# Kernel tuning notes

Measured on AMD Instinct MI355X. Metric: run time of the kernel, lower is better.

## Reference

```python
import jax, jax.numpy as jnp
import numpy as np

B, HID = 32768, 128
NU = 0.49                 # poisson_ratio default
LAM_PHYS, LAM_EL = 0.1, 0.05
EPS = 1e-7


def setup_inputs() -> dict:
    key = jax.random.key(0)
    ks = jax.random.split(key, 8)
    def w(k, shape, fan_in):
        return jax.random.normal(k, shape, jnp.float32) / np.float32(np.sqrt(fan_in))
    return {
        "coords": jax.random.normal(ks[0], (B, 3), jnp.float32),
        "target_labels": jax.random.uniform(ks[1], (B, 1), jnp.float32),
        "target_stiffness": jax.random.uniform(ks[2], (B, 1), jnp.float32) * 10.0,
        "W1": w(ks[3], (3, HID), 3), "b1": jnp.zeros((HID,), jnp.float32),
        "W2": w(ks[4], (HID, HID), HID), "b2": jnp.zeros((HID,), jnp.float32),
        "Wp": w(ks[5], (HID, 1), HID), "bp": jnp.zeros((1,), jnp.float32),
        "Ws": w(ks[6], (HID, 1), HID), "bs": jnp.zeros((1,), jnp.float32),
        "Wd": w(ks[7], (HID, 3), HID), "bd": jnp.zeros((3,), jnp.float32),
    }


def reference(coords, target_labels, target_stiffness,
              W1, b1, W2, b2, Wp, bp, Ws, bs, Wd, bd):
    def feats(x):  # x: (...,3) -> (...,HID)
        h = jnp.tanh(x @ W1 + b1)
        return jnp.tanh(h @ W2 + b2)

    h = feats(coords)                                   # (B,HID)
    prediction = jax.nn.sigmoid(h @ Wp + bp)            # (B,1)
    stiffness = jax.nn.softplus(h @ Ws + bs)            # (B,1) Young's modulus E

    # displacement field u(x): R^3 -> R^3, pointwise
    def disp_fn(x):  # (3,) -> (3,)
        return feats(x) @ Wd + bd

    # Per-point Hessian H[b,i,j,k] = d2 u_i / dx_j dx_k  (B,3,3,3)
    Hm = jax.vmap(jax.jacfwd(jax.jacfwd(disp_fn)))(coords)
    laplacian = jnp.einsum('bijj->bi', Hm)              # (B,3) lap(u_i)
    grad_div = jnp.einsum('biik->bk', Hm)               # (B,3) grad(div u)

    # Lame parameters from E (matches torch code incl. nu_denom clamp)
    mu = stiffness / (2.0 * (1.0 + NU))
    nu_denom = max(1.0 - 2.0 * NU, 1e-5)
    lmbda = stiffness * NU / ((1.0 + NU) * nu_denom)
    residual = mu * laplacian + (lmbda + mu) * grad_div  # (B,3)
    phys_loss = jnp.mean(jnp.sum(residual ** 2, axis=-1))

    # BCE on clamped prediction/labels
    p = jnp.clip(prediction, EPS, 1.0 - EPS)
    t = jnp.clip(target_labels, 0.0, 1.0)
    bce = -jnp.mean(t * jnp.log(p) + (1.0 - t) * jnp.log(1.0 - p))
    data_loss = bce + 0.5 * jnp.mean((stiffness - target_stiffness) ** 2)

    elastic_loss = jnp.mean(jax.nn.relu(-stiffness) + jax.nn.relu(stiffness - 15.0))

    total = data_loss + LAM_PHYS * phys_loss + LAM_EL * elastic_loss
    raw_losses = jnp.stack([data_loss, phys_loss, elastic_loss])
    return total, raw_losses
```

## Files before the change

kernel.cpp:

```cpp
#include <hip/hip_runtime.h>
#include <math.h>

#define HIDN 128
#define NPTS 32768
#define PTS_PER_BLK 16
#define NBLK (NPTS / PTS_PER_BLK)

#define MU_COEF 0.33557046979865773f
#define LM_COEF 16.442953020134228f

typedef float f32x4  __attribute__((ext_vector_type(4)));
typedef short bf16x8 __attribute__((ext_vector_type(8)));


__device__ __forceinline__ unsigned short f2bf(float f) {
    unsigned u = __builtin_bit_cast(unsigned, f);
    u += 0x7fffu + ((u >> 16) & 1u);
    return (unsigned short)(u >> 16);
}

__device__ __forceinline__ float tanh_fast(float x) {
    float e = __builtin_amdgcn_exp2f(x * 2.885390081777927f);
    return 1.0f - 2.0f * __builtin_amdgcn_rcpf(e + 1.0f);
}

__global__ void prep_kernel(const float* __restrict__ W1,
                            const float* __restrict__ b1,
                            const float* __restrict__ W2,
                            float* __restrict__ ws)
{
    float* accum = ws;
    float* tab   = ws + 128;
    unsigned short* W2bf = (unsigned short*)(ws + 2048);
    int tid = blockIdx.x * blockDim.x + threadIdx.x;
    if (tid < 8) accum[tid] = 0.0f;
    if (tid < HIDN) {
        float w0 = W1[0 * HIDN + tid];
        float w1 = W1[1 * HIDN + tid];
        float w2 = W1[2 * HIDN + tid];
        float* t = tab + tid * 12;
        t[0] = w0; t[1] = w1; t[2] = w2; t[3] = b1[tid];
        t[4] = w0 * w0; t[5] = w0 * w1; t[6] = w0 * w2;
        t[7] = w1 * w1; t[8] = w1 * w2; t[9] = w2 * w2;
        t[10] = 0.0f; t[11] = 0.0f;
    }
    for (int i = tid; i < HIDN * HIDN; i += gridDim.x * blockDim.x) {
        int m = i >> 7, h = i & 127;
        W2bf[m * HIDN + h] = f2bf(W2[h * HIDN + m]);
    }
}

__global__ __launch_bounds__(256, 3) void pinn_main(
    const float* __restrict__ coords,
    const float* __restrict__ labels,
    const float* __restrict__ tstiff,
    const float* __restrict__ b2,
    const float* __restrict__ Wp, const float* __restrict__ bp,
    const float* __restrict__ Wsv, const float* __restrict__ bs,
    const float* __restrict__ Wd,
    const float* __restrict__ ws_ro,
    float* __restrict__ accum)
{
    const float* tab = ws_ro + 128;
    const unsigned short* W2bf = (const unsigned short*)(ws_ro + 2048);

    __shared__ __align__(16) char smem[43584];
    unsigned short* A  = (unsigned short*)smem;
    float*          red  = (float*)smem;
    float*          red2 = (float*)(smem + 43520);

    const int tid  = threadIdx.x;
    const int wave = __builtin_amdgcn_readfirstlane(tid >> 6);
    const int lane = tid & 63;
    const int blk  = blockIdx.x;

    {
        const int b  = tid & 15;
        const int hc = tid >> 4;
        const int h0 = hc * 8;
        const int gb = blk * PTS_PER_BLK + b;
        const float x0 = coords[gb * 3 + 0];
        const float x1 = coords[gb * 3 + 1];
        const float x2 = coords[gb * 3 + 2];
        unsigned pk[10][4];
#pragma unroll
        for (int i = 0; i < 8; ++i) {
            const float* t = tab + (h0 + i) * 12;
            float z = fmaf(x0, t[0], fmaf(x1, t[1], fmaf(x2, t[2], t[3])));
            float a  = tanh_fast(z);
            float g  = fmaf(-a, a, 1.0f);
            float ag = a * g;
            float c[10];
            c[0] = a;
            c[1] = g * t[0]; c[2] = g * t[1]; c[3] = g * t[2];
            c[4] = ag * t[4]; c[5] = ag * t[5]; c[6] = ag * t[6];
            c[7] = ag * t[7]; c[8] = ag * t[8]; c[9] = ag * t[9];
#pragma unroll
            for (int ch = 0; ch < 10; ++ch) {
                unsigned v = f2bf(c[ch]);
                if ((i & 1) == 0) pk[ch][i >> 1] = v;
                else              pk[ch][i >> 1] |= v << 16;
            }
        }
#pragma unroll
        for (int ch = 0; ch < 10; ++ch) {
            uint4* dst = (uint4*)(A + ch * (16 * 136) + b * 136 + h0);
            *dst = make_uint4(pk[ch][0], pk[ch][1], pk[ch][2], pk[ch][3]);
        }
    }
    __syncthreads();

    const int l = lane & 15;
    const int q = lane >> 4;

    f32x4 acc[10][2] = {};
#pragma unroll
    for (int ks = 0; ks < 4; ++ks) {
        const int hk = ks * 32 + q * 8;
        bf16x8 bfr[2];
#pragma unroll
        for (int mt = 0; mt < 2; ++mt) {
            const int m = wave * 32 + mt * 16 + l;
            bfr[mt] = *(const bf16x8*)(W2bf + m * HIDN + hk);
        }
#pragma unroll
        for (int ch = 0; ch < 10; ++ch) {
            bf16x8 afr = *(const bf16x8*)(A + ch * (16 * 136) + l * 136 + hk);
            acc[ch][0] = __builtin_amdgcn_mfma_f32_16x16x32_bf16(afr, bfr[0], acc[ch][0], 0, 0, 0);
            acc[ch][1] = __builtin_amdgcn_mfma_f32_16x16x32_bf16(afr, bfr[1], acc[ch][1], 0, 0, 0);
        }
    }

    float sum[4][8] = {};
#pragma unroll
    for (int mt = 0; mt < 2; ++mt) {
        const int m = wave * 32 + mt * 16 + l;
        const float wd0 = Wd[m * 3 + 0];
        const float wd1 = Wd[m * 3 + 1];
        const float wd2 = Wd[m * 3 + 2];
        const float wp  = Wp[m];
        const float wsv = Wsv[m];
        const float b2v = b2[m];
#pragma unroll
        for (int r = 0; r < 4; ++r) {
            const float z2 = acc[0][mt][r] + b2v;
            const float a2 = tanh_fast(z2);
            const float g2 = fmaf(-a2, a2, 1.0f);
            const float d2 = -2.0f * a2 * g2;
            const float t0 = acc[1][mt][r], t1 = acc[2][mt][r], t2 = acc[3][mt][r];
            const float q00 = acc[4][mt][r], q01 = acc[5][mt][r], q02 = acc[6][mt][r];
            const float q11 = acc[7][mt][r], q12 = acc[8][mt][r], q22 = acc[9][mt][r];
            const float qtr = q00 + q11 + q22;
            const float tt  = t0 * t0 + t1 * t1 + t2 * t2;
            const float Lm  = fmaf(-2.0f * g2, qtr, d2 * tt);
            const float wt  = wd0 * t0 + wd1 * t1 + wd2 * t2;
            const float m2g2 = -2.0f * g2;
            const float dwt  = d2 * wt;
            const float r0 = wd0 * q00 + wd1 * q01 + wd2 * q02;
            const float r1 = wd0 * q01 + wd1 * q11 + wd2 * q12;
            const float r2 = wd0 * q02 + wd1 * q12 + wd2 * q22;
            sum[r][0] += wp  * a2;
            sum[r][1] += wsv * a2;
            sum[r][2] += wd0 * Lm;
            sum[r][3] += wd1 * Lm;
            sum[r][4] += wd2 * Lm;
            sum[r][5] += m2g2 * r0 + dwt * t0;
            sum[r][6] += m2g2 * r1 + dwt * t1;
            sum[r][7] += m2g2 * r2 + dwt * t2;
        }
    }
    __syncthreads();

#pragma unroll
    for (int r = 0; r < 4; ++r) {
        const int b = q * 4 + r;
        const int slot = wave * 16 + l;
        float4* dst = (float4*)(red + (b * 64 + slot) * 8);
        dst[0] = make_float4(sum[r][0], sum[r][1], sum[r][2], sum[r][3]);
        dst[1] = make_float4(sum[r][4], sum[r][5], sum[r][6], sum[r][7]);
    }
    __syncthreads();

    {
        const int b  = tid >> 4;
        const int l2 = tid & 15;
        float v[8] = {};
#pragma unroll
        for (int w = 0; w < 4; ++w) {
            const float4* src = (const float4*)(red + (b * 64 + w * 16 + l2) * 8);
            float4 p0 = src[0], p1 = src[1];
            v[0] += p0.x; v[1] += p0.y; v[2] += p0.z; v[3] += p0.w;
            v[4] += p1.x; v[5] += p1.y; v[6] += p1.z; v[7] += p1.w;
        }
#pragma unroll
        for (int k = 0; k < 8; ++k) {
            v[k] += __shfl_xor(v[k], 1);
            v[k] += __shfl_xor(v[k], 2);
            v[k] += __shfl_xor(v[k], 4);
            v[k] += __shfl_xor(v[k], 8);
        }
        float bce_t = 0.f, sq_t = 0.f, phys_t = 0.f, el_t = 0.f;
        if (l2 == 0) {
            const int gb = blk * PTS_PER_BLK + b;
            const float fzp = v[0] + bp[0];
            const float fzs = v[1] + bs[0];
            float pred = 1.0f / (1.0f + expf(-fzp));
            pred = fminf(fmaxf(pred, 1e-7f), 1.0f - 1e-7f);
            const float E = fmaxf(fzs, 0.0f) + log1pf(expf(-fabsf(fzs)));
            const float mu = E * MU_COEF;
            const float cc = E * LM_COEF + mu;
            const float rr0 = mu * v[2] + cc * v[5];
            const float rr1 = mu * v[3] + cc * v[6];
            const float rr2 = mu * v[4] + cc * v[7];
            phys_t = rr0 * rr0 + rr1 * rr1 + rr2 * rr2;
            float tl = labels[gb];
            tl = fminf(fmaxf(tl, 0.0f), 1.0f);
            bce_t = -(tl * logf(pred) + (1.0f - tl) * logf(1.0f - pred));
            const float dsv = E - tstiff[gb];
            sq_t = dsv * dsv;
            el_t = fmaxf(-E, 0.0f) + fmaxf(E - 15.0f, 0.0f);
        }
#pragma unroll
        for (int m = 16; m < 64; m <<= 1) {
            bce_t  += __shfl_xor(bce_t, m);
            sq_t   += __shfl_xor(sq_t, m);
            phys_t += __shfl_xor(phys_t, m);
            el_t   += __shfl_xor(el_t, m);
        }
        if (lane == 0) {
            red2[wave * 4 + 0] = bce_t;
            red2[wave * 4 + 1] = sq_t;
            red2[wave * 4 + 2] = phys_t;
            red2[wave * 4 + 3] = el_t;
        }
    }
    __syncthreads();
    if (tid < 4) {
        float s = red2[0 * 4 + tid] + red2[1 * 4 + tid] + red2[2 * 4 + tid] + red2[3 * 4 + tid];
        atomicAdd(accum + tid, s);
    }
}

__global__ void finalize_kernel(const float* __restrict__ accum,
                                float* __restrict__ out)
{
    if (threadIdx.x == 0 && blockIdx.x == 0) {
        const float invB = 1.0f / (float)NPTS;
        const float bce  = accum[0] * invB;
        const float data = bce + 0.5f * accum[1] * invB;
        const float phys = accum[2] * invB;
        const float el   = accum[3] * invB;
        out[0] = data + 0.1f * phys + 0.05f * el;
        out[1] = data;
        out[2] = phys;
        out[3] = el;
    }
}

extern "C" void kernel_launch(void* const* d_in, const int* in_sizes, int n_in,
                              void* d_out, int out_size, void* d_ws, size_t ws_size,
                              hipStream_t stream)
{
    const float* coords = (const float*)d_in[0];
    const float* labels = (const float*)d_in[1];
    const float* tstiff = (const float*)d_in[2];
    const float* W1  = (const float*)d_in[3];
    const float* b1  = (const float*)d_in[4];
    const float* W2  = (const float*)d_in[5];
    const float* b2  = (const float*)d_in[6];
    const float* Wp  = (const float*)d_in[7];
    const float* bp  = (const float*)d_in[8];
    const float* Wsv = (const float*)d_in[9];
    const float* bs  = (const float*)d_in[10];
    const float* Wd  = (const float*)d_in[11];

    float* ws  = (float*)d_ws;
    float* out = (float*)d_out;

    prep_kernel<<<64, 256, 0, stream>>>(W1, b1, W2, ws);
    pinn_main<<<NBLK, 256, 0, stream>>>(coords, labels, tstiff, b2,
                                        Wp, bp, Wsv, bs, Wd, ws, ws);
    finalize_kernel<<<1, 64, 0, stream>>>(ws, out);
}
```

Measured before the change: 117.1 us.

## Fold first-layer weights into W2 variants to shrink per-point MFMA A operands

Moves the W1-dependent factors (w_j, |w|^2, Wd·w products) into nine precomputed bf16 B matrices, so each point needs only three A channels (a, g, a*g) instead of ten. The main kernel now handles 64 points per block, uses an XOR-swizzled LDS layout, loops over output column chunks, and fuses finalization into the last block via an atomic counter. This cuts per-point activation work and LDS traffic but adds more MFMAs per point (9 vs 10 per m-tile with larger tiles) and more global B-matrix reads, and it lowers occupancy to 2 blocks per CU. Extra bf16 rounding of the folded weights may change accuracy.

```diff
diff --git a/kernel.cpp b/kernel.cpp
--- a/kernel.cpp
+++ b/kernel.cpp
@@ -3,8 +3,8 @@
 
 #define HIDN 128
 #define NPTS 32768
-#define PTS_PER_BLK 16
-#define NBLK (NPTS / PTS_PER_BLK)
+#define PTSB 64
+#define NBLK (NPTS / PTSB)
 
 #define MU_COEF 0.33557046979865773f
 #define LM_COEF 16.442953020134228f
@@ -27,30 +27,39 @@
 __global__ void prep_kernel(const float* __restrict__ W1,
                             const float* __restrict__ b1,
                             const float* __restrict__ W2,
+                            const float* __restrict__ Wd,
                             float* __restrict__ ws)
 {
-    float* accum = ws;
-    float* tab   = ws + 128;
-    unsigned short* W2bf = (unsigned short*)(ws + 2048);
-    int tid = blockIdx.x * blockDim.x + threadIdx.x;
-    if (tid < 8) accum[tid] = 0.0f;
-    if (tid < HIDN) {
-        float w0 = W1[0 * HIDN + tid];
-        float w1 = W1[1 * HIDN + tid];
-        float w2 = W1[2 * HIDN + tid];
-        float* t = tab + tid * 12;
-        t[0] = w0; t[1] = w1; t[2] = w2; t[3] = b1[tid];
-        t[4] = w0 * w0; t[5] = w0 * w1; t[6] = w0 * w2;
-        t[7] = w1 * w1; t[8] = w1 * w2; t[9] = w2 * w2;
-        t[10] = 0.0f; t[11] = 0.0f;
-    }
-    for (int i = tid; i < HIDN * HIDN; i += gridDim.x * blockDim.x) {
-        int m = i >> 7, h = i & 127;
-        W2bf[m * HIDN + h] = f2bf(W2[h * HIDN + m]);
-    }
-}
-
-__global__ __launch_bounds__(256, 3) void pinn_main(
+    const int idx = blockIdx.x * blockDim.x + threadIdx.x;
+    const int h = idx & 127;
+    const int m = idx >> 7;
+    if (idx < 8) ws[idx] = 0.0f;
+    const float w0 = W1[0 * HIDN + h];
+    const float w1 = W1[1 * HIDN + h];
+    const float w2 = W1[2 * HIDN + h];
+    if (idx < 128) {
+        float4* tab4 = (float4*)(ws + 16);
+        tab4[h] = make_float4(w0, w1, w2, b1[h]);
+    }
+    const float W2v = W2[h * HIDN + m];
+    const float kap = w0 * Wd[m * 3 + 0] + w1 * Wd[m * 3 + 1] + w2 * Wd[m * 3 + 2];
+    const float s   = w0 * w0 + w1 * w1 + w2 * w2;
+    unsigned short* BM = (unsigned short*)((char*)ws + 4096);
+    const int o = m * HIDN + h;
+    BM[0 * 16384 + o] = f2bf(W2v);
+    BM[1 * 16384 + o] = f2bf(W2v * w0);
+    BM[2 * 16384 + o] = f2bf(W2v * w1);
+    BM[3 * 16384 + o] = f2bf(W2v * w2);
+    BM[4 * 16384 + o] = f2bf(W2v * kap);
+    BM[5 * 16384 + o] = f2bf(W2v * s);
+    BM[6 * 16384 + o] = f2bf(W2v * w0 * kap);
+    BM[7 * 16384 + o] = f2bf(W2v * w1 * kap);
+    BM[8 * 16384 + o] = f2bf(W2v * w2 * kap);
+}
+
+__constant__ int AIDX_[9] = {0, 1, 1, 1, 1, 2, 2, 2, 2};
+
+__global__ __launch_bounds__(256, 2) void pinn_main(
     const float* __restrict__ coords,
     const float* __restrict__ labels,
     const float* __restrict__ tstiff,
@@ -59,201 +68,206 @@
     const float* __restrict__ Wsv, const float* __restrict__ bs,
     const float* __restrict__ Wd,
     const float* __restrict__ ws_ro,
-    float* __restrict__ accum)
+    float* __restrict__ accum,
+    float* __restrict__ out)
 {
-    const float* tab = ws_ro + 128;
-    const unsigned short* W2bf = (const unsigned short*)(ws_ro + 2048);
-
-    __shared__ __align__(16) char smem[43584];
+    const float4* tab4 = (const float4*)(ws_ro + 16);
+    const unsigned short* BM = (const unsigned short*)((const char*)ws_ro + 4096);
+
+    __shared__ __align__(16) char smem[57344];
     unsigned short* A  = (unsigned short*)smem;
-    float*          red  = (float*)smem;
-    float*          red2 = (float*)(smem + 43520);
-
-    const int tid  = threadIdx.x;
-    const int wave = __builtin_amdgcn_readfirstlane(tid >> 6);
-    const int lane = tid & 63;
+    float*          red = (float*)(smem + 49152);
+
+    const int t    = threadIdx.x;
+    const int w    = __builtin_amdgcn_readfirstlane(t >> 6);
+    const int lane = t & 63;
+    const int l    = lane & 15;
+    const int q    = lane >> 4;
     const int blk  = blockIdx.x;
 
     {
-        const int b  = tid & 15;
-        const int hc = tid >> 4;
-        const int h0 = hc * 8;
-        const int gb = blk * PTS_PER_BLK + b;
+        float4* r4 = (float4*)red;
+        r4[t * 2 + 0] = make_float4(0.f, 0.f, 0.f, 0.f);
+        r4[t * 2 + 1] = make_float4(0.f, 0.f, 0.f, 0.f);
+    }
+
+    {
+        const int b  = t & 63;
+        const int gb = blk * PTSB + b;
         const float x0 = coords[gb * 3 + 0];
         const float x1 = coords[gb * 3 + 1];
         const float x2 = coords[gb * 3 + 2];
-        unsigned pk[10][4];
-#pragma unroll
-        for (int i = 0; i < 8; ++i) {
-            const float* t = tab + (h0 + i) * 12;
-            float z = fmaf(x0, t[0], fmaf(x1, t[1], fmaf(x2, t[2], t[3])));
-            float a  = tanh_fast(z);
-            float g  = fmaf(-a, a, 1.0f);
-            float ag = a * g;
-            float c[10];
-            c[0] = a;
-            c[1] = g * t[0]; c[2] = g * t[1]; c[3] = g * t[2];
-            c[4] = ag * t[4]; c[5] = ag * t[5]; c[6] = ag * t[6];
-            c[7] = ag * t[7]; c[8] = ag * t[8]; c[9] = ag * t[9];
-#pragma unroll
-            for (int ch = 0; ch < 10; ++ch) {
-                unsigned v = f2bf(c[ch]);
-                if ((i & 1) == 0) pk[ch][i >> 1] = v;
-                else              pk[ch][i >> 1] |= v << 16;
-            }
-        }
-#pragma unroll
-        for (int ch = 0; ch < 10; ++ch) {
-            uint4* dst = (uint4*)(A + ch * (16 * 136) + b * 136 + h0);
-            *dst = make_uint4(pk[ch][0], pk[ch][1], pk[ch][2], pk[ch][3]);
+#pragma unroll
+        for (int i = 0; i < 4; ++i) {
+            const int c = w * 4 + i;
+            unsigned pk[3][4];
+#pragma unroll
+            for (int hh = 0; hh < 8; ++hh) {
+                float4 tv = tab4[c * 8 + hh];
+                float z  = fmaf(x0, tv.x, fmaf(x1, tv.y, fmaf(x2, tv.z, tv.w)));
+                float a  = tanh_fast(z);
+                float g  = fmaf(-a, a, 1.0f);
+                float ag = a * g;
+                unsigned va = f2bf(a), vg = f2bf(g), vag = f2bf(ag);
+                if ((hh & 1) == 0) { pk[0][hh >> 1] = va; pk[1][hh >> 1] = vg; pk[2][hh >> 1] = vag; }
+                else { pk[0][hh >> 1] |= va << 16; pk[1][hh >> 1] |= vg << 16; pk[2][hh >> 1] |= vag << 16; }
+            }
+            const int dst = b * 128 + ((c ^ (b & 15)) * 8);
+#pragma unroll
+            for (int ch = 0; ch < 3; ++ch)
+                *(uint4*)(A + ch * 8192 + dst) = make_uint4(pk[ch][0], pk[ch][1], pk[ch][2], pk[ch][3]);
         }
     }
     __syncthreads();
 
-    const int l = lane & 15;
-    const int q = lane >> 4;
-
-    f32x4 acc[10][2] = {};
-#pragma unroll
-    for (int ks = 0; ks < 4; ++ks) {
-        const int hk = ks * 32 + q * 8;
-        bf16x8 bfr[2];
-#pragma unroll
-        for (int mt = 0; mt < 2; ++mt) {
-            const int m = wave * 32 + mt * 16 + l;
-            bfr[mt] = *(const bf16x8*)(W2bf + m * HIDN + hk);
-        }
-#pragma unroll
-        for (int ch = 0; ch < 10; ++ch) {
-            bf16x8 afr = *(const bf16x8*)(A + ch * (16 * 136) + l * 136 + hk);
-            acc[ch][0] = __builtin_amdgcn_mfma_f32_16x16x32_bf16(afr, bfr[0], acc[ch][0], 0, 0, 0);
-            acc[ch][1] = __builtin_amdgcn_mfma_f32_16x16x32_bf16(afr, bfr[1], acc[ch][1], 0, 0, 0);
-        }
-    }
-
-    float sum[4][8] = {};
-#pragma unroll
-    for (int mt = 0; mt < 2; ++mt) {
-        const int m = wave * 32 + mt * 16 + l;
-        const float wd0 = Wd[m * 3 + 0];
-        const float wd1 = Wd[m * 3 + 1];
-        const float wd2 = Wd[m * 3 + 2];
-        const float wp  = Wp[m];
-        const float wsv = Wsv[m];
-        const float b2v = b2[m];
-#pragma unroll
-        for (int r = 0; r < 4; ++r) {
-            const float z2 = acc[0][mt][r] + b2v;
-            const float a2 = tanh_fast(z2);
-            const float g2 = fmaf(-a2, a2, 1.0f);
-            const float d2 = -2.0f * a2 * g2;
-            const float t0 = acc[1][mt][r], t1 = acc[2][mt][r], t2 = acc[3][mt][r];
-            const float q00 = acc[4][mt][r], q01 = acc[5][mt][r], q02 = acc[6][mt][r];
-            const float q11 = acc[7][mt][r], q12 = acc[8][mt][r], q22 = acc[9][mt][r];
-            const float qtr = q00 + q11 + q22;
-            const float tt  = t0 * t0 + t1 * t1 + t2 * t2;
-            const float Lm  = fmaf(-2.0f * g2, qtr, d2 * tt);
-            const float wt  = wd0 * t0 + wd1 * t1 + wd2 * t2;
-            const float m2g2 = -2.0f * g2;
-            const float dwt  = d2 * wt;
-            const float r0 = wd0 * q00 + wd1 * q01 + wd2 * q02;
-            const float r1 = wd0 * q01 + wd1 * q11 + wd2 * q12;
-            const float r2 = wd0 * q02 + wd1 * q12 + wd2 * q22;
-            sum[r][0] += wp  * a2;
-            sum[r][1] += wsv * a2;
-            sum[r][2] += wd0 * Lm;
-            sum[r][3] += wd1 * Lm;
-            sum[r][4] += wd2 * Lm;
-            sum[r][5] += m2g2 * r0 + dwt * t0;
-            sum[r][6] += m2g2 * r1 + dwt * t1;
-            sum[r][7] += m2g2 * r2 + dwt * t2;
+#pragma unroll
+    for (int rt = 0; rt < 2; ++rt) {
+        float pv[2][4][8];
+#pragma unroll
+        for (int a_ = 0; a_ < 2; ++a_)
+#pragma unroll
+            for (int b_ = 0; b_ < 4; ++b_)
+#pragma unroll
+                for (int k_ = 0; k_ < 8; ++k_) pv[a_][b_][k_] = 0.f;
+
+#pragma unroll
+        for (int mc = 0; mc < 2; ++mc) {
+            const int m = mc * 64 + w * 16 + l;
+            const float wd0 = Wd[m * 3 + 0];
+            const float wd1 = Wd[m * 3 + 1];
+            const float wd2 = Wd[m * 3 + 2];
+            const float wpv = Wp[m];
+            const float wsvv = Wsv[m];
+            const float b2v = b2[m];
+
+            f32x4 acc[9][2] = {};
+#pragma unroll
+            for (int ks = 0; ks < 4; ++ks) {
+                bf16x8 af[3][2];
+#pragma unroll
+                for (int Mt = 0; Mt < 2; ++Mt) {
+                    const int br = rt * 32 + Mt * 16 + l;
+                    const int sw = ((ks * 4 + q) ^ l) * 8;
+#pragma unroll
+                    for (int ac = 0; ac < 3; ++ac)
+                        af[ac][Mt] = *(const bf16x8*)(A + ac * 8192 + br * 128 + sw);
+                }
+                bf16x8 bfm[9];
+#pragma unroll
+                for (int ch = 0; ch < 9; ++ch)
+                    bfm[ch] = *(const bf16x8*)(BM + ch * 16384 + m * 128 + ks * 32 + q * 8);
+#pragma unroll
+                for (int ch = 0; ch < 9; ++ch) {
+                    const int ai = (ch == 0) ? 0 : ((ch <= 4) ? 1 : 2);
+                    acc[ch][0] = __builtin_amdgcn_mfma_f32_16x16x32_bf16(af[ai][0], bfm[ch], acc[ch][0], 0, 0, 0);
+                    acc[ch][1] = __builtin_amdgcn_mfma_f32_16x16x32_bf16(af[ai][1], bfm[ch], acc[ch][1], 0, 0, 0);
+                }
+            }
+#pragma unroll
+            for (int Mt = 0; Mt < 2; ++Mt) {
+#pragma unroll
+                for (int r = 0; r < 4; ++r) {
+                    const float z2 = acc[0][Mt][r] + b2v;
+                    const float a2 = tanh_fast(z2);
+                    const float g2 = fmaf(-a2, a2, 1.0f);
+                    const float d2 = -2.0f * a2 * g2;
+                    const float t0 = acc[1][Mt][r], t1 = acc[2][Mt][r], t2 = acc[3][Mt][r];
+                    const float wt = acc[4][Mt][r];
+                    const float qtr = acc[5][Mt][r];
+                    const float r0 = acc[6][Mt][r], r1 = acc[7][Mt][r], r2 = acc[8][Mt][r];
+                    const float Lm = fmaf(-2.0f * g2, qtr, d2 * (t0 * t0 + t1 * t1 + t2 * t2));
+                    const float m2g2 = -2.0f * g2;
+                    const float dwt  = d2 * wt;
+                    pv[Mt][r][0] += wpv * a2;
+                    pv[Mt][r][1] += wsvv * a2;
+                    pv[Mt][r][2] += wd0 * Lm;
+                    pv[Mt][r][3] += wd1 * Lm;
+                    pv[Mt][r][4] += wd2 * Lm;
+                    pv[Mt][r][5] += m2g2 * r0 + dwt * t0;
+                    pv[Mt][r][6] += m2g2 * r1 + dwt * t1;
+                    pv[Mt][r][7] += m2g2 * r2 + dwt * t2;
+                }
+            }
+        }
+#pragma unroll
+        for (int Mt = 0; Mt < 2; ++Mt) {
+#pragma unroll
+            for (int r = 0; r < 4; ++r) {
+                float v[8];
+#pragma unroll
+                for (int k = 0; k < 8; ++k) {
+                    float x = pv[Mt][r][k];
+                    x += __shfl_xor(x, 1);
+                    x += __shfl_xor(x, 2);
+                    x += __shfl_xor(x, 4);
+                    x += __shfl_xor(x, 8);
+                    v[k] = x;
+                }
+                if (l == 0) {
+                    const int bb = rt * 32 + Mt * 16 + q * 4 + r;
+                    float* dst = red + (w * 64 + bb) * 8;
+#pragma unroll
+                    for (int k = 0; k < 8; ++k) dst[k] += v[k];
+                }
+            }
         }
     }
     __syncthreads();
 
-#pragma unroll
-    for (int r = 0; r < 4; ++r) {
-        const int b = q * 4 + r;
-        const int slot = wave * 16 + l;
-        float4* dst = (float4*)(red + (b * 64 + slot) * 8);
-        dst[0] = make_float4(sum[r][0], sum[r][1], sum[r][2], sum[r][3]);
-        dst[1] = make_float4(sum[r][4], sum[r][5], sum[r][6], sum[r][7]);
-    }
-    __syncthreads();
-
-    {
-        const int b  = tid >> 4;
-        const int l2 = tid & 15;
+    if (t < 64) {
+        const int b = t;
         float v[8] = {};
 #pragma unroll
-        for (int w = 0; w < 4; ++w) {
-            const float4* src = (const float4*)(red + (b * 64 + w * 16 + l2) * 8);
+        for (int ww = 0; ww < 4; ++ww) {
+            const float4* src = (const float4*)(red + (ww * 64 + b) * 8);
             float4 p0 = src[0], p1 = src[1];
             v[0] += p0.x; v[1] += p0.y; v[2] += p0.z; v[3] += p0.w;
             v[4] += p1.x; v[5] += p1.y; v[6] += p1.z; v[7] += p1.w;
         }
-#pragma unroll
-        for (int k = 0; k < 8; ++k) {
-            v[k] += __shfl_xor(v[k], 1);
-            v[k] += __shfl_xor(v[k], 2);
-            v[k] += __shfl_xor(v[k], 4);
-            v[k] += __shfl_xor(v[k], 8);
-        }
-        float bce_t = 0.f, sq_t = 0.f, phys_t = 0.f, el_t = 0.f;
-        if (l2 == 0) {
-            const int gb = blk * PTS_PER_BLK + b;
-            const float fzp = v[0] + bp[0];
-            const float fzs = v[1] + bs[0];
-            float pred = 1.0f / (1.0f + expf(-fzp));
-            pred = fminf(fmaxf(pred, 1e-7f), 1.0f - 1e-7f);
-            const float E = fmaxf(fzs, 0.0f) + log1pf(expf(-fabsf(fzs)));
-            const float mu = E * MU_COEF;
-            const float cc = E * LM_COEF + mu;
-            const float rr0 = mu * v[2] + cc * v[5];
-            const float rr1 = mu * v[3] + cc * v[6];
-            const float rr2 = mu * v[4] + cc * v[7];
-            phys_t = rr0 * rr0 + rr1 * rr1 + rr2 * rr2;
-            float tl = labels[gb];
-            tl = fminf(fmaxf(tl, 0.0f), 1.0f);
-            bce_t = -(tl * logf(pred) + (1.0f - tl) * logf(1.0f - pred));
-            const float dsv = E - tstiff[gb];
-            sq_t = dsv * dsv;
-            el_t = fmaxf(-E, 0.0f) + fmaxf(E - 15.0f, 0.0f);
-        }
-#pragma unroll
-        for (int m = 16; m < 64; m <<= 1) {
-            bce_t  += __shfl_xor(bce_t, m);
-            sq_t   += __shfl_xor(sq_t, m);
-            phys_t += __shfl_xor(phys_t, m);
-            el_t   += __shfl_xor(el_t, m);
-        }
-        if (lane == 0) {
-            red2[wave * 4 + 0] = bce_t;
-            red2[wave * 4 + 1] = sq_t;
-            red2[wave * 4 + 2] = phys_t;
-            red2[wave * 4 + 3] = el_t;
-        }
-    }
-    __syncthreads();
-    if (tid < 4) {
-        float s = red2[0 * 4 + tid] + red2[1 * 4 + tid] + red2[2 * 4 + tid] + red2[3 * 4 + tid];
-        atomicAdd(accum + tid, s);
-    }
-}
-
-__global__ void finalize_kernel(const float* __restrict__ accum,
-                                float* __restrict__ out)
-{
-    if (threadIdx.x == 0 && blockIdx.x == 0) {
-        const float invB = 1.0f / (float)NPTS;
-        const float bce  = accum[0] * invB;
-        const float data = bce + 0.5f * accum[1] * invB;
-        const float phys = accum[2] * invB;
-        const float el   = accum[3] * invB;
-        out[0] = data + 0.1f * phys + 0.05f * el;
-        out[1] = data;
-        out[2] = phys;
-        out[3] = el;
+        const int gb = blk * PTSB + b;
+        const float fzp = v[0] + bp[0];
+        const float fzs = v[1] + bs[0];
+        float pred = 1.0f / (1.0f + expf(-fzp));
+        pred = fminf(fmaxf(pred, 1e-7f), 1.0f - 1e-7f);
+        const float E = fmaxf(fzs, 0.0f) + log1pf(expf(-fabsf(fzs)));
+        const float mu = E * MU_COEF;
+        const float cc = E * LM_COEF + mu;
+        const float rr0 = mu * v[2] + cc * v[5];
+        const float rr1 = mu * v[3] + cc * v[6];
+        const float rr2 = mu * v[4] + cc * v[7];
+        float phys_t = rr0 * rr0 + rr1 * rr1 + rr2 * rr2;
+        float tl = labels[gb];
+        tl = fminf(fmaxf(tl, 0.0f), 1.0f);
+        float bce_t = -(tl * logf(pred) + (1.0f - tl) * logf(1.0f - pred));
+        const float dsv = E - tstiff[gb];
+        float sq_t = dsv * dsv;
+        float el_t = fmaxf(-E, 0.0f) + fmaxf(E - 15.0f, 0.0f);
+#pragma unroll
+        for (int off = 1; off < 64; off <<= 1) {
+            bce_t  += __shfl_xor(bce_t, off);
+            sq_t   += __shfl_xor(sq_t, off);
+            phys_t += __shfl_xor(phys_t, off);
+            el_t   += __shfl_xor(el_t, off);
+        }
+        if (t == 0) {
+            atomicAdd(accum + 0, bce_t);
+            atomicAdd(accum + 1, sq_t);
+            atomicAdd(accum + 2, phys_t);
+            atomicAdd(accum + 3, el_t);
+            __threadfence();
+            int old = atomicAdd((int*)(accum + 7), 1);
+            if (old == NBLK - 1) {
+                const float invB = 1.0f / (float)NPTS;
+                const float bce  = atomicAdd(accum + 0, 0.0f) * invB;
+                const float data = bce + 0.5f * atomicAdd(accum + 1, 0.0f) * invB;
+                const float phys = atomicAdd(accum + 2, 0.0f) * invB;
+                const float el   = atomicAdd(accum + 3, 0.0f) * invB;
+                out[0] = data + 0.1f * phys + 0.05f * el;
+                out[1] = data;
+                out[2] = phys;
+                out[3] = el;
+            }
+        }
     }
 }
 
@@ -277,8 +291,7 @@
     float* ws  = (float*)d_ws;
     float* out = (float*)d_out;
 
-    prep_kernel<<<64, 256, 0, stream>>>(W1, b1, W2, ws);
+    prep_kernel<<<64, 256, 0, stream>>>(W1, b1, W2, Wd, ws);
     pinn_main<<<NBLK, 256, 0, stream>>>(coords, labels, tstiff, b2,
-                                        Wp, bp, Wsv, bs, Wd, ws, ws);
-    finalize_kernel<<<1, 64, 0, stream>>>(ws, out);
-}
+                                        Wp, bp, Wsv, bs, Wd, ws, ws, out);
+}
```

After: 160.9 us. +37.4%, slower.
